# Kernel tuning notes

Hardware: AMD Instinct MI355X
Metric: run time of the kernel (lower is better)

## Reference

```python
import jax, jax.numpy as jnp
import numpy as np

N, E = 50000, 200000
EMB_ATOM, EMB_EDGE = 256, 512
IN_SIZE = 2 * EMB_ATOM + EMB_EDGE  # 1024


def setup_inputs() -> dict:
    key = jax.random.key(0)
    k_h, k_m, k_i, k_j, k_w = jax.random.split(key, 5)
    h = jax.random.normal(k_h, (N, EMB_ATOM), dtype=jnp.float32)
    m_ij = jax.random.normal(k_m, (E, EMB_EDGE), dtype=jnp.float32)
    idx_i = jax.random.randint(k_i, (E,), 0, N, dtype=jnp.int64)
    idx_j = jax.random.randint(k_j, (E,), 0, N, dtype=jnp.int64)
    # bias-free Dense weight, stored as (in, out) for x @ W
    W = jax.random.normal(k_w, (IN_SIZE, EMB_EDGE), dtype=jnp.float32) * (1.0 / np.sqrt(IN_SIZE))
    return {"h": h, "m_ij": m_ij, "idx_i": idx_i, "idx_j": idx_j, "W": W}


def reference(h, m_ij, idx_i, idx_j, W):
    h_i = h[idx_i]                                   # (E, emb_atom)
    h_j = h[idx_j]                                   # (E, emb_atom)
    x = jnp.concatenate([h_i, h_j, m_ij], axis=-1)   # (E, 2*emb_atom + emb_edge)
    out = x @ W                                      # (E, emb_edge), bias-free Dense
    return jax.nn.silu(out)
```

## Files before the change

### kernel.cpp

```cpp
#include <hip/hip_runtime.h>
#include <hip/hip_bf16.h>
#include <math.h>

#define EMB_ATOM 256
#define EMB_EDGE 512
#define K_TOT    1024

typedef __attribute__((ext_vector_type(8))) short bf16x8;
typedef __attribute__((ext_vector_type(4))) float f32x4;
typedef struct { unsigned short x, y, z, w; } us4;

static __device__ __forceinline__ unsigned short f2bf(float f) {
  union { float f; unsigned u; } x; x.f = f;
  unsigned r = x.u + 0x7fffu + ((x.u >> 16) & 1u);
  return (unsigned short)(r >> 16);
}
static __device__ __forceinline__ float bf2f(unsigned short b) {
  union { unsigned u; float f; } x; x.u = ((unsigned)b) << 16; return x.f;
}
static __device__ __forceinline__ us4 f4bf(float4 v) {
  us4 o; o.x = f2bf(v.x); o.y = f2bf(v.y); o.z = f2bf(v.z); o.w = f2bf(v.w); return o;
}
static __device__ __forceinline__ bf16x8 cvt8(float4 a, float4 b) {
  union { bf16x8 v; __hip_bfloat162 h[4]; } u;
  u.h[0] = __float22bfloat162_rn(make_float2(a.x, a.y));
  u.h[1] = __float22bfloat162_rn(make_float2(a.z, a.w));
  u.h[2] = __float22bfloat162_rn(make_float2(b.x, b.y));
  u.h[3] = __float22bfloat162_rn(make_float2(b.z, b.w));
  return u.v;
}
static __device__ __forceinline__ void gload_lds16(const void* g, void* l) {
  __builtin_amdgcn_global_load_lds(
      (const __attribute__((address_space(1))) unsigned int*)g,
      (__attribute__((address_space(3))) unsigned int*)l, 16, 0, 0);
}
static __device__ __forceinline__ float silu_f(float x) { return x / (1.f + __expf(-x)); }

__global__ __launch_bounds__(256) void cvt_h_kernel(const float* __restrict__ h,
                                                    unsigned short* __restrict__ hb, int n4) {
  int i = blockIdx.x * 256 + threadIdx.x;
  if (i >= n4) return;
  const float4 v = ((const float4*)h)[i];
  ((us4*)hb)[i] = f4bf(v);
}

__global__ __launch_bounds__(256) void cvt_wh_kernel(const float* __restrict__ W,
                                                     unsigned short* __restrict__ Wt_h) {
  int o = blockIdx.x * 256 + threadIdx.x;
  int c = o >> 8, k = o & 255;
  float v = (c < 512) ? W[(size_t)k * EMB_EDGE + c]
                      : W[(size_t)(256 + k) * EMB_EDGE + (c - 512)];
  Wt_h[o] = f2bf(v);
}

__global__ __launch_bounds__(256) void cvt_wm_kernel(const float* __restrict__ W,
                                                     unsigned short* __restrict__ Wt_m) {
  int o = blockIdx.x * 256 + threadIdx.x;
  int c = o >> 9, k = o & 511;
  Wt_m[o] = f2bf(W[(size_t)(512 + k) * EMB_EDGE + c]);
}

__global__ __launch_bounds__(256) void hgemm_kernel(
    const unsigned short* __restrict__ hb,
    const unsigned short* __restrict__ Wt_h,
    unsigned short* __restrict__ H12, int N)
{
  __shared__ unsigned short As[2][128 * 64];
  __shared__ unsigned short Bs[2][128 * 64];
  const int bn = blockIdx.x;
  const int bm = blockIdx.y;
  const int row0 = bm * 128;
  const int tid = threadIdx.x, wave = tid >> 6, lane = tid & 63;
  const int srow = lane >> 3;
  const int schunk = ((lane & 7) ^ srow) * 8;

  size_t abase[4]; size_t bbase[4];
#pragma unroll
  for (int i = 0; i < 4; ++i) {
    int r = wave * 32 + i * 8 + srow;
    int e = row0 + r; if (e >= N) e = N - 1;
    abase[i] = (size_t)e * EMB_ATOM;
    bbase[i] = (size_t)(bn * 128 + r) * EMB_ATOM;
  }

  const int wr = wave >> 1, wc = wave & 1, fr = lane & 15, fq = lane >> 4;
  const int fs = fr & 7;

  f32x4 acc[4][4];
#pragma unroll
  for (int m = 0; m < 4; ++m)
#pragma unroll
    for (int n = 0; n < 4; ++n) acc[m][n] = (f32x4)0.f;

#pragma unroll
  for (int i = 0; i < 4; ++i) {
    gload_lds16(hb + abase[i] + schunk,   &As[0][(wave * 32 + i * 8) * 64 + lane * 8]);
    gload_lds16(Wt_h + bbase[i] + schunk, &Bs[0][(wave * 32 + i * 8) * 64 + lane * 8]);
  }
  __syncthreads();

  int cur = 0;
  for (int kt = 0; kt < 4; ++kt) {
    int nxt = cur ^ 1;
    if (kt < 3) {
      int kk = (kt + 1) * 64;
#pragma unroll
      for (int i = 0; i < 4; ++i) {
        gload_lds16(hb + abase[i] + kk + schunk,   &As[nxt][(wave * 32 + i * 8) * 64 + lane * 8]);
        gload_lds16(Wt_h + bbase[i] + kk + schunk, &Bs[nxt][(wave * 32 + i * 8) * 64 + lane * 8]);
      }
    }
#pragma unroll
    for (int ks = 0; ks < 2; ++ks) {
      bf16x8 a[4], b[4];
#pragma unroll
      for (int m = 0; m < 4; ++m)
        a[m] = *(const bf16x8*)(&As[cur][(wr * 64 + m * 16 + fr) * 64 + (((ks * 4 + fq) ^ fs) << 3)]);
#pragma unroll
      for (int n = 0; n < 4; ++n)
        b[n] = *(const bf16x8*)(&Bs[cur][(wc * 64 + n * 16 + fr) * 64 + (((ks * 4 + fq) ^ fs) << 3)]);
#pragma unroll
      for (int m = 0; m < 4; ++m)
#pragma unroll
        for (int n = 0; n < 4; ++n)
          acc[m][n] = __builtin_amdgcn_mfma_f32_16x16x32_bf16(a[m], b[n], acc[m][n], 0, 0, 0);
    }
    __syncthreads();
    cur = nxt;
  }

#pragma unroll
  for (int m = 0; m < 4; ++m) {
    int er0 = row0 + wr * 64 + m * 16 + fq * 4;
#pragma unroll
    for (int n = 0; n < 4; ++n) {
      int col = bn * 128 + wc * 64 + n * 16 + fr;
      f32x4 v = acc[m][n];
#pragma unroll
      for (int j = 0; j < 4; ++j) {
        int e = er0 + j;
        if (e < N) H12[(size_t)e * 1024 + col] = f2bf(v[j]);
      }
    }
  }
}

__global__ __launch_bounds__(512, 4) void mgemm_kernel(
    const float* __restrict__ m_ij,
    const int* __restrict__ idx_i,
    const int* __restrict__ idx_j,
    const unsigned short* __restrict__ Wt_m,
    const unsigned short* __restrict__ H12,
    float* __restrict__ out, int E, int nbm)
{
  __shared__ __align__(16) float          As[2][128 * 32];
  __shared__ __align__(16) unsigned short Bs[2][256 * 32];

  int b  = blockIdx.x;
  int bm = (b & 7) + (b >> 4) * 8;
  int bn = (b >> 3) & 1;
  if (bm >= nbm) return;
  const int row0 = bm * 128;
  const int tid = threadIdx.x, wave = tid >> 6, lane = tid & 63;
  const int fr = lane & 15, fq = lane >> 4;
  const int wr = wave >> 2, wc = wave & 3;

  const float* asrc[2];
  const unsigned short* bsrc[2];
#pragma unroll
  for (int i = 0; i < 2; ++i) {
    int flat = i * 512 + tid;
    int ar = flat >> 3, ac = flat & 7;
    int e = row0 + ar; if (e >= E) e = E - 1;
    asrc[i] = m_ij + (size_t)e * EMB_EDGE + ((ac ^ (ar & 7)) << 2);
    int br = flat >> 2, bc = flat & 3;
    bsrc[i] = Wt_m + (size_t)(bn * 256 + br) * 512 + ((bc ^ (br & 3)) << 3);
  }
  const unsigned abase = wave * 64 * 4;
  const unsigned bbase = wave * 64 * 8;

  f32x4 acc[4][4];
#pragma unroll
  for (int m = 0; m < 4; ++m)
#pragma unroll
    for (int n = 0; n < 4; ++n) acc[m][n] = (f32x4)0.f;

#pragma unroll
  for (int i = 0; i < 2; ++i) {
    gload_lds16(asrc[i], &As[0][i * 512 * 4 + abase]);
    gload_lds16(bsrc[i], &Bs[0][i * 512 * 8 + bbase]);
  }
  __syncthreads();

  for (int kt = 0; kt < 16; ++kt) {
    const int cur = kt & 1;
    if (kt < 15) {
      const int kk = (kt + 1) * 32;
#pragma unroll
      for (int i = 0; i < 2; ++i) {
        gload_lds16(asrc[i] + kk, &As[cur ^ 1][i * 512 * 4 + abase]);
        gload_lds16(bsrc[i] + kk, &Bs[cur ^ 1][i * 512 * 8 + bbase]);
      }
    }
    bf16x8 bfr[4];
#pragma unroll
    for (int n = 0; n < 4; ++n) {
      const int row = wc * 64 + n * 16 + fr;
      bfr[n] = *(const bf16x8*)(&Bs[cur][row * 32 + ((fq ^ (row & 3)) << 3)]);
    }
#pragma unroll
    for (int m = 0; m < 4; ++m) {
      const int row = wr * 64 + m * 16 + fr;
      float4 c0 = *(const float4*)(&As[cur][row * 32 + (((fq * 2) ^ (row & 7)) << 2)]);
      float4 c1 = *(const float4*)(&As[cur][row * 32 + (((fq * 2 + 1) ^ (row & 7)) << 2)]);
      bf16x8 afr = cvt8(c0, c1);
#pragma unroll
      for (int n = 0; n < 4; ++n)
        acc[m][n] = __builtin_amdgcn_mfma_f32_16x16x32_bf16(afr, bfr[n], acc[m][n], 0, 0, 0);
    }
    __syncthreads();
  }

#pragma unroll
  for (int m = 0; m < 4; ++m) {
#pragma unroll
    for (int j = 0; j < 4; ++j) {
      int e = row0 + wr * 64 + m * 16 + fq * 4 + j;
      if (e < E) {
        size_t gi = (size_t)idx_i[e] * 1024;
        size_t gj = (size_t)idx_j[e] * 1024 + 512;
#pragma unroll
        for (int n = 0; n < 4; ++n) {
          int col = bn * 256 + wc * 64 + n * 16 + fr;
          float x = acc[m][n][j] + bf2f(H12[gi + col]) + bf2f(H12[gj + col]);
          out[(size_t)e * EMB_EDGE + col] = silu_f(x);
        }
      }
    }
  }
}

__global__ __launch_bounds__(256) void cvt_wt_kernel(const float* __restrict__ W,
                                                     unsigned short* __restrict__ Wt) {
  int o = blockIdx.x * 256 + threadIdx.x;
  int n = o >> 10, k = o & 1023;
  Wt[o] = f2bf(W[(size_t)k * EMB_EDGE + n]);
}

__global__ __launch_bounds__(256) void gemm_gather_kernel(
    const unsigned short* __restrict__ hb,
    const float* __restrict__ m_ij,
    const int* __restrict__ idx_i,
    const int* __restrict__ idx_j,
    const unsigned short* __restrict__ Wt,
    float* __restrict__ out, int E)
{
  __shared__ unsigned short As[128 * 64];
  __shared__ unsigned short Bs[128 * 64];
  const int bn = blockIdx.x, bm = blockIdx.y;
  const int tid = threadIdx.x, wave = tid >> 6, lane = tid & 63;
  const int row0 = bm * 128;
  const int srow = lane >> 3, scol = (lane & 7) * 8;
  int arow[4], aii[4], ajj[4];
#pragma unroll
  for (int i = 0; i < 4; ++i) {
    int r = wave * 32 + i * 8 + srow;
    int e = row0 + r; if (e >= E) e = E - 1;
    arow[i] = r; aii[i] = idx_i[e]; ajj[i] = idx_j[e];
  }
  const int wr = wave >> 1, wc = wave & 1, fr = lane & 15, fq = lane >> 4;
  f32x4 acc[4][4];
#pragma unroll
  for (int m = 0; m < 4; ++m)
#pragma unroll
    for (int n = 0; n < 4; ++n) acc[m][n] = (f32x4)0.f;
  for (int kt = 0; kt < 16; ++kt) {
    __syncthreads();
#pragma unroll
    for (int i = 0; i < 4; ++i) {
      int nl = wave * 32 + i * 8 + srow;
      gload_lds16(Wt + (size_t)(bn * 128 + nl) * K_TOT + kt * 64 + scol, &Bs[nl * 64 + scol]);
    }
    if (kt < 8) {
      const int kh = (kt & 3) * 64;
#pragma unroll
      for (int i = 0; i < 4; ++i) {
        int idx = (kt < 4) ? aii[i] : ajj[i];
        gload_lds16(hb + (size_t)idx * EMB_ATOM + kh + scol, &As[arow[i] * 64 + scol]);
      }
    } else {
      const int kk = (kt - 8) * 64;
#pragma unroll
      for (int it = 0; it < 8; ++it) {
        int flat = it * 1024 + tid * 4;
        int r = flat >> 6, c = flat & 63;
        int e = row0 + r; if (e >= E) e = E - 1;
        const float4 v = *(const float4*)(m_ij + (size_t)e * EMB_EDGE + kk + c);
        *(us4*)(&As[r * 64 + c]) = f4bf(v);
      }
    }
    __syncthreads();
#pragma unroll
    for (int ks = 0; ks < 2; ++ks) {
      bf16x8 a[4], b[4];
#pragma unroll
      for (int m = 0; m < 4; ++m)
        a[m] = *(const bf16x8*)(&As[(wr * 64 + m * 16 + fr) * 64 + ks * 32 + fq * 8]);
#pragma unroll
      for (int n = 0; n < 4; ++n)
        b[n] = *(const bf16x8*)(&Bs[(wc * 64 + n * 16 + fr) * 64 + ks * 32 + fq * 8]);
#pragma unroll
      for (int m = 0; m < 4; ++m)
#pragma unroll
        for (int n = 0; n < 4; ++n)
          acc[m][n] = __builtin_amdgcn_mfma_f32_16x16x32_bf16(a[m], b[n], acc[m][n], 0, 0, 0);
    }
  }
#pragma unroll
  for (int m = 0; m < 4; ++m) {
    int er0 = row0 + wr * 64 + m * 16 + fq * 4;
#pragma unroll
    for (int n = 0; n < 4; ++n) {
      int col = bn * 128 + wc * 64 + n * 16 + fr;
      f32x4 v = acc[m][n];
#pragma unroll
      for (int j = 0; j < 4; ++j) {
        int e = er0 + j;
        if (e < E) out[(size_t)e * EMB_EDGE + col] = silu_f(v[j]);
      }
    }
  }
}

extern "C" void kernel_launch(void* const* d_in, const int* in_sizes, int n_in,
                              void* d_out, int out_size, void* d_ws, size_t ws_size,
                              hipStream_t stream) {
  const float* h    = (const float*)d_in[0];
  const float* m_ij = (const float*)d_in[1];
  const int*   ii   = (const int*)d_in[2];
  const int*   jj   = (const int*)d_in[3];
  const float* W    = (const float*)d_in[4];
  float* out = (float*)d_out;

  const int hsz = in_sizes[0];
  const int N   = hsz / EMB_ATOM;
  const int E   = in_sizes[2];

  unsigned short* hb   = (unsigned short*)d_ws;
  unsigned short* Wt_h = hb + hsz;
  unsigned short* Wt_m = Wt_h + 1024 * 256;
  unsigned short* H12  = Wt_m + 512 * 512;
  size_t need = ((size_t)hsz + 1024 * 256 + 512 * 512 + (size_t)N * 1024) * 2;

  if (ws_size >= need) {
    cvt_h_kernel<<<(hsz / 4 + 255) / 256, 256, 0, stream>>>(h, hb, hsz / 4);
    cvt_wh_kernel<<<1024, 256, 0, stream>>>(W, Wt_h);
    cvt_wm_kernel<<<1024, 256, 0, stream>>>(W, Wt_m);
    int nbmh = (N + 127) / 128;
    hgemm_kernel<<<dim3(8, nbmh), 256, 0, stream>>>(hb, Wt_h, H12, N);
    int nbm  = (E + 127) / 128;
    int ngrp = (nbm + 7) / 8;
    mgemm_kernel<<<ngrp * 16, 512, 0, stream>>>(m_ij, ii, jj, Wt_m, H12, out, E, nbm);
  } else {
    unsigned short* Wt  = (unsigned short*)d_ws;
    unsigned short* hbf = Wt + 512 * 1024;
    cvt_wt_kernel<<<(512 * 1024) / 256, 256, 0, stream>>>(W, Wt);
    cvt_h_kernel<<<(hsz / 4 + 255) / 256, 256, 0, stream>>>(h, hbf, hsz / 4);
    dim3 grid(4, (E + 127) / 128);
    gemm_gather_kernel<<<grid, 256, 0, stream>>>(hbf, m_ij, ii, jj, Wt, out, E);
  }
}
```

Before: 470.2 us.

## Enlarge mgemm tile to 256x512 with 1024-thread blocks, drop double buffering

The m_ij GEMM now uses one 1024-thread block per 256 edge rows covering all 512 output columns, so each m_ij tile is read from global memory once instead of twice across two column blocks. The LDS double buffer is replaced by single-buffered load, sync, compute, sync. This halves A traffic and doubles per-wave accumulators, but load and compute no longer overlap and register pressure rises to 128 accumulator floats per thread.

```diff
diff --git a/kernel.cpp b/kernel.cpp
--- a/kernel.cpp
+++ b/kernel.cpp
@@ -145,22 +145,19 @@
   }
 }
 
-__global__ __launch_bounds__(512, 4) void mgemm_kernel(
+__global__ __launch_bounds__(1024, 2) void mgemm_kernel(
     const float* __restrict__ m_ij,
     const int* __restrict__ idx_i,
     const int* __restrict__ idx_j,
     const unsigned short* __restrict__ Wt_m,
     const unsigned short* __restrict__ H12,
-    float* __restrict__ out, int E, int nbm)
+    float* __restrict__ out, int E)
 {
-  __shared__ __align__(16) float          As[2][128 * 32];
-  __shared__ __align__(16) unsigned short Bs[2][256 * 32];
-
-  int b  = blockIdx.x;
-  int bm = (b & 7) + (b >> 4) * 8;
-  int bn = (b >> 3) & 1;
-  if (bm >= nbm) return;
-  const int row0 = bm * 128;
+  __shared__ __align__(16) float          As[256 * 32];
+  __shared__ __align__(16) unsigned short Bs[512 * 32];
+
+  const int bm = blockIdx.x;
+  const int row0 = bm * 256;
   const int tid = threadIdx.x, wave = tid >> 6, lane = tid & 63;
   const int fr = lane & 15, fq = lane >> 4;
   const int wr = wave >> 2, wc = wave & 3;
@@ -169,54 +166,46 @@
   const unsigned short* bsrc[2];
 #pragma unroll
   for (int i = 0; i < 2; ++i) {
-    int flat = i * 512 + tid;
+    int flat = i * 1024 + tid;
     int ar = flat >> 3, ac = flat & 7;
     int e = row0 + ar; if (e >= E) e = E - 1;
     asrc[i] = m_ij + (size_t)e * EMB_EDGE + ((ac ^ (ar & 7)) << 2);
     int br = flat >> 2, bc = flat & 3;
-    bsrc[i] = Wt_m + (size_t)(bn * 256 + br) * 512 + ((bc ^ (br & 3)) << 3);
-  }
-  const unsigned abase = wave * 64 * 4;
-  const unsigned bbase = wave * 64 * 8;
-
-  f32x4 acc[4][4];
+    bsrc[i] = Wt_m + (size_t)br * 512 + ((bc ^ ((br >> 1) & 3)) << 3);
+  }
+
+  f32x4 acc[4][8];
 #pragma unroll
   for (int m = 0; m < 4; ++m)
 #pragma unroll
-    for (int n = 0; n < 4; ++n) acc[m][n] = (f32x4)0.f;
-
-#pragma unroll
-  for (int i = 0; i < 2; ++i) {
-    gload_lds16(asrc[i], &As[0][i * 512 * 4 + abase]);
-    gload_lds16(bsrc[i], &Bs[0][i * 512 * 8 + bbase]);
-  }
-  __syncthreads();
+    for (int n = 0; n < 8; ++n) acc[m][n] = (f32x4)0.f;
 
   for (int kt = 0; kt < 16; ++kt) {
-    const int cur = kt & 1;
-    if (kt < 15) {
-      const int kk = (kt + 1) * 32;
-#pragma unroll
-      for (int i = 0; i < 2; ++i) {
-        gload_lds16(asrc[i] + kk, &As[cur ^ 1][i * 512 * 4 + abase]);
-        gload_lds16(bsrc[i] + kk, &Bs[cur ^ 1][i * 512 * 8 + bbase]);
-      }
-    }
-    bf16x8 bfr[4];
-#pragma unroll
-    for (int n = 0; n < 4; ++n) {
-      const int row = wc * 64 + n * 16 + fr;
-      bfr[n] = *(const bf16x8*)(&Bs[cur][row * 32 + ((fq ^ (row & 3)) << 3)]);
-    }
-#pragma unroll
-    for (int m = 0; m < 4; ++m) {
-      const int row = wr * 64 + m * 16 + fr;
-      float4 c0 = *(const float4*)(&As[cur][row * 32 + (((fq * 2) ^ (row & 7)) << 2)]);
-      float4 c1 = *(const float4*)(&As[cur][row * 32 + (((fq * 2 + 1) ^ (row & 7)) << 2)]);
-      bf16x8 afr = cvt8(c0, c1);
-#pragma unroll
-      for (int n = 0; n < 4; ++n)
-        acc[m][n] = __builtin_amdgcn_mfma_f32_16x16x32_bf16(afr, bfr[n], acc[m][n], 0, 0, 0);
+    const int kk = kt * 32;
+#pragma unroll
+    for (int i = 0; i < 2; ++i) {
+      gload_lds16(asrc[i] + kk, &As[(i * 1024 + tid) * 4]);
+      gload_lds16(bsrc[i] + kk, &Bs[(i * 1024 + tid) * 8]);
+    }
+    __syncthreads();
+
+    {
+      bf16x8 bfr[8];
+#pragma unroll
+      for (int n = 0; n < 8; ++n) {
+        const int row = wc * 128 + n * 16 + fr;
+        bfr[n] = *(const bf16x8*)(&Bs[row * 32 + ((fq ^ ((row >> 1) & 3)) << 3)]);
+      }
+#pragma unroll
+      for (int m = 0; m < 4; ++m) {
+        const int row = wr * 64 + m * 16 + fr;
+        float4 c0 = *(const float4*)(&As[row * 32 + (((fq * 2) ^ (row & 7)) << 2)]);
+        float4 c1 = *(const float4*)(&As[row * 32 + (((fq * 2 + 1) ^ (row & 7)) << 2)]);
+        bf16x8 afr = cvt8(c0, c1);
+#pragma unroll
+        for (int n = 0; n < 8; ++n)
+          acc[m][n] = __builtin_amdgcn_mfma_f32_16x16x32_bf16(afr, bfr[n], acc[m][n], 0, 0, 0);
+      }
     }
     __syncthreads();
   }
@@ -230,8 +219,8 @@
         size_t gi = (size_t)idx_i[e] * 1024;
         size_t gj = (size_t)idx_j[e] * 1024 + 512;
 #pragma unroll
-        for (int n = 0; n < 4; ++n) {
-          int col = bn * 256 + wc * 64 + n * 16 + fr;
+        for (int n = 0; n < 8; ++n) {
+          int col = wc * 128 + n * 16 + fr;
           float x = acc[m][n][j] + bf2f(H12[gi + col]) + bf2f(H12[gj + col]);
           out[(size_t)e * EMB_EDGE + col] = silu_f(x);
         }
@@ -358,9 +347,8 @@
     cvt_wm_kernel<<<1024, 256, 0, stream>>>(W, Wt_m);
     int nbmh = (N + 127) / 128;
     hgemm_kernel<<<dim3(8, nbmh), 256, 0, stream>>>(hb, Wt_h, H12, N);
-    int nbm  = (E + 127) / 128;
-    int ngrp = (nbm + 7) / 8;
-    mgemm_kernel<<<ngrp * 16, 512, 0, stream>>>(m_ij, ii, jj, Wt_m, H12, out, E, nbm);
+    int nbm = (E + 255) / 256;
+    mgemm_kernel<<<nbm, 1024, 0, stream>>>(m_ij, ii, jj, Wt_m, H12, out, E);
   } else {
     unsigned short* Wt  = (unsigned short*)d_ws;
     unsigned short* hbf = Wt + 512 * 1024;
```

After: 1.776 ms. +277.8%, slower.
